# Kernel optimization log

Measured on AMD Instinct MI355X. Metric: run time of the kernel, lower is better.

The kernel has to match this reference:

```python
import jax, jax.numpy as jnp
import numpy as np

H = 16
D_MODEL = 1024
D_K = D_MODEL // H  # 64


def setup_inputs() -> dict:
    key = jax.random.key(0)
    ks = jax.random.split(key, 11)
    B, S = 4, 2048
    scale_in = 1.0 / np.sqrt(D_MODEL)
    inp = {
        "q": jax.random.normal(ks[0], (B, S, D_MODEL), jnp.float32),
        "k": jax.random.normal(ks[1], (B, S, D_MODEL), jnp.float32),
        "v": jax.random.normal(ks[2], (B, S, D_MODEL), jnp.float32),
        # linear params, [in, out] layout (y = x @ W + b)
        "Wq": jax.random.normal(ks[3], (D_MODEL, D_MODEL), jnp.float32) * scale_in,
        "bq": jnp.zeros((D_MODEL,), jnp.float32),
        "Wk": jax.random.normal(ks[4], (D_MODEL, D_K), jnp.float32) * scale_in,
        "bk": jnp.zeros((D_K,), jnp.float32),
        "Wv": jax.random.normal(ks[5], (D_MODEL, D_K), jnp.float32) * scale_in,
        "bv": jnp.zeros((D_K,), jnp.float32),
        "Wo": jax.random.normal(ks[6], (D_MODEL, D_MODEL), jnp.float32) * scale_in,
        "bo": jnp.zeros((D_MODEL,), jnp.float32),
    }
    return inp


def reference(q, k, v, Wq, bq, Wk, bk, Wv, bv, Wo, bo):
    B, S, _ = q.shape
    # projections
    qh = (q @ Wq + bq).reshape(B, S, H, D_K).transpose(0, 2, 1, 3)  # [B,H,S,dk]
    kh = k @ Wk + bk  # [B,S,dk]  single shared K head
    vh = v @ Wv + bv  # [B,S,dk]  single shared V head
    # scaled dot-product attention with broadcast KV head
    scores = jnp.einsum("bhqd,bkd->bhqk", qh, kh) / jnp.sqrt(jnp.float32(D_K))
    p = jax.nn.softmax(scores, axis=-1)  # [B,H,S,S]
    out = jnp.einsum("bhqk,bkd->bhqd", p, vh)  # [B,H,S,dk]
    out = out.transpose(0, 2, 1, 3).reshape(B, S, H * D_K)
    return out @ Wo + bo
```

## Files before the change

kernel.cpp:

```cpp
#include <hip/hip_runtime.h>
#include <hip/hip_bf16.h>

typedef unsigned short u16;
typedef unsigned int u32;
typedef float f32x4 __attribute__((ext_vector_type(4)));
typedef float f32x16 __attribute__((ext_vector_type(16)));
typedef u32 u32x4 __attribute__((ext_vector_type(4)));
typedef __bf16 bf16x8 __attribute__((ext_vector_type(8)));

#define DEVI static __device__ __forceinline__

static constexpr float QK_SCALE = 0.125f * 1.44269504088896340736f;

DEVI u16 bfbits(float f) { __bf16 h = (__bf16)f; return __builtin_bit_cast(u16, h); }
DEVI u32 pk2(float lo, float hi) { return (u32)bfbits(lo) | ((u32)bfbits(hi) << 16); }
DEVI void lswap(u32& a, u32& b) { asm("v_permlane32_swap_b32 %0, %1" : "+v"(a), "+v"(b)); }

typedef unsigned int uint_g __attribute__((address_space(1)));
typedef unsigned int uint_l __attribute__((address_space(3)));

DEVI void gl_lds16(const void* g, void* l) {
  __builtin_amdgcn_global_load_lds((const uint_g*)g, (uint_l*)l, 16, 0, 0);
}

__global__ __launch_bounds__(256) void cvt_f32_bf16(const float* __restrict__ x,
                                                    u16* __restrict__ y, int n4) {
  int i = blockIdx.x * blockDim.x + threadIdx.x;
  int stride = gridDim.x * blockDim.x;
  for (; i < n4; i += stride) {
    float4 v = ((const float4*)x)[i];
    ushort4 o;
    o.x = bfbits(v.x); o.y = bfbits(v.y); o.z = bfbits(v.z); o.w = bfbits(v.w);
    ((ushort4*)y)[i] = o;
  }
}

__global__ __launch_bounds__(256) void wtrans(const float* __restrict__ W,
                                              u16* __restrict__ WT, int K, int N) {
  __shared__ float t[32][33];
  int k0 = blockIdx.x * 32, n0 = blockIdx.y * 32;
  int tx = threadIdx.x & 31, ty = threadIdx.x >> 5;
#pragma unroll
  for (int i = 0; i < 4; ++i)
    t[ty + i * 8][tx] = W[(size_t)(k0 + ty + i * 8) * N + n0 + tx];
  __syncthreads();
#pragma unroll
  for (int i = 0; i < 4; ++i)
    WT[(size_t)(n0 + ty + i * 8) * K + k0 + tx] = bfbits(t[tx][ty + i * 8]);
}

template <int BM, int BN, int WM, int WN, int EPI>
__global__ __launch_bounds__(256) void gemm_bt(const u16* __restrict__ A,
                                               const u16* __restrict__ BT,
                                               const float* __restrict__ bias,
                                               void* __restrict__ out,
                                               int M, int N, int K) {
  constexpr int WROWS = BM / WM, WCOLS = BN / WN;
  constexpr int RT = WROWS / 16, CT = WCOLS / 16;
  __shared__ u16 Alds[BM * 64];
  __shared__ u16 Blds[BN * 64];
  const int tid = threadIdx.x, wave = tid >> 6, lane = tid & 63;
  const int lr = lane & 15, lg = lane >> 4;
  const int wr = wave / WN, wc = wave % WN;
  const int m0 = blockIdx.y * BM, n0 = blockIdx.x * BN;

  f32x4 acc[RT][CT] = {};
  const int nkt = K >> 6;
  for (int kt = 0; kt < nkt; ++kt) {
    const int k0 = kt * 64;
#pragma unroll
    for (int j = 0; j < BM / 32; ++j) {
      int row = j * 32 + (tid >> 3);
      int cel = ((tid & 7) * 8) ^ ((row & 7) << 3);
      gl_lds16(A + (size_t)(m0 + row) * K + k0 + cel,
               (char*)Alds + (j * 256 + wave * 64) * 16);
    }
#pragma unroll
    for (int j = 0; j < BN / 32; ++j) {
      int row = j * 32 + (tid >> 3);
      int cel = ((tid & 7) * 8) ^ ((row & 7) << 3);
      gl_lds16(BT + (size_t)(n0 + row) * K + k0 + cel,
               (char*)Blds + (j * 256 + wave * 64) * 16);
    }
    __syncthreads();
#pragma unroll
    for (int ks = 0; ks < 2; ++ks) {
      bf16x8 af[RT], bfv[CT];
#pragma unroll
      for (int rt = 0; rt < RT; ++rt) {
        int r = wr * WROWS + rt * 16 + lr;
        af[rt] = *(const bf16x8*)&Alds[r * 64 + ((ks * 32 + lg * 8) ^ ((r & 7) << 3))];
      }
#pragma unroll
      for (int ct = 0; ct < CT; ++ct) {
        int r = wc * WCOLS + ct * 16 + lr;
        bfv[ct] = *(const bf16x8*)&Blds[r * 64 + ((ks * 32 + lg * 8) ^ ((r & 7) << 3))];
      }
#pragma unroll
      for (int rt = 0; rt < RT; ++rt)
#pragma unroll
        for (int ct = 0; ct < CT; ++ct)
          acc[rt][ct] = __builtin_amdgcn_mfma_f32_16x16x32_bf16(af[rt], bfv[ct], acc[rt][ct], 0, 0, 0);
    }
    __syncthreads();
  }
#pragma unroll
  for (int ct = 0; ct < CT; ++ct) {
    int n = n0 + wc * WCOLS + ct * 16 + lr;
    float bv = bias[n];
#pragma unroll
    for (int rt = 0; rt < RT; ++rt) {
#pragma unroll
      for (int r = 0; r < 4; ++r) {
        int m = m0 + wr * WROWS + rt * 16 + lg * 4 + r;
        float v = acc[rt][ct][r] + bv;
        if constexpr (EPI == 0) {
          ((float*)out)[(size_t)m * N + n] = v;
        } else if constexpr (EPI == 1) {
          ((u16*)out)[(size_t)m * N + n] = bfbits(v);
        } else if constexpr (EPI == 2) {
          ((u16*)out)[(size_t)m * N + n] = bfbits(v * QK_SCALE);
        } else {
          int bb = m >> 11, s2 = m & 2047;
          ((u16*)out)[((size_t)bb * 64 + n) * 2048 + s2] = bfbits(v);
        }
      }
    }
  }
}

__global__ __launch_bounds__(256, 3) void attn(const u16* __restrict__ qh,
                                               const u16* __restrict__ kh,
                                               const u16* __restrict__ vhT,
                                               u16* __restrict__ att) {
  const int b = blockIdx.z;
  const int tid = threadIdx.x;
  const int wave = tid >> 6, lane = tid & 63;
  const int lq = lane & 31, hi = lane >> 5;
  const int h = blockIdx.y * 4 + wave;
  const int q0 = blockIdx.x * 32;

  __shared__ char KV[2][16384];

  const u16* Qb = qh + (size_t)(b * 2048 + q0) * 1024 + h * 64;
  const u16* Kb = kh + (size_t)b * 2048 * 64;
  const u16* Vb = vhT + (size_t)b * 64 * 2048;

  auto stage = [&](int buf, int kt) {
    char* Lk = KV[buf];
    char* Lv = KV[buf] + 8192;
#pragma unroll
    for (int j = 0; j < 2; ++j) {
      int row = j * 32 + (tid >> 3);
      int cel = ((tid & 7) * 8) ^ ((row & 7) << 3);
      gl_lds16(Kb + (size_t)(kt * 64 + row) * 64 + cel, Lk + j * 4096 + wave * 1024);
      gl_lds16(Vb + (size_t)row * 2048 + kt * 64 + cel, Lv + j * 4096 + wave * 1024);
    }
  };

  bf16x8 qf[4];
#pragma unroll
  for (int ks = 0; ks < 4; ++ks)
    qf[ks] = *(const bf16x8*)(Qb + (size_t)lq * 1024 + ks * 16 + hi * 8);

  f32x16 acc0 = {}, acc1 = {};
  float m = -__builtin_inff(), l = 0.f;

  stage(0, 0);
  __syncthreads();

#pragma unroll 1
  for (int kt = 0; kt < 32; ++kt) {
    const int cur = kt & 1;
    if (kt < 31) stage(cur ^ 1, kt + 1);
    const char* Lk = KV[cur];
    const char* Lv = KV[cur] + 8192;
    f32x16 sc0 = {}, sc1 = {};
    {
      bf16x8 ka[2][4];
#pragma unroll
      for (int t = 0; t < 2; ++t)
#pragma unroll
        for (int ks = 0; ks < 4; ++ks) {
          int row = t * 32 + lq;
          ka[t][ks] = *(const bf16x8*)(Lk + row * 128 + ((ks * 32 + hi * 16) ^ ((row & 7) << 4)));
        }
      __builtin_amdgcn_s_setprio(1);
#pragma unroll
      for (int ks = 0; ks < 4; ++ks)
        sc0 = __builtin_amdgcn_mfma_f32_32x32x16_bf16(ka[0][ks], qf[ks], sc0, 0, 0, 0);
#pragma unroll
      for (int ks = 0; ks < 4; ++ks)
        sc1 = __builtin_amdgcn_mfma_f32_32x32x16_bf16(ka[1][ks], qf[ks], sc1, 0, 0, 0);
      __builtin_amdgcn_s_setprio(0);
    }
    bf16x8 va[2][2][2];
#pragma unroll
    for (int dt = 0; dt < 2; ++dt)
#pragma unroll
      for (int t = 0; t < 2; ++t)
#pragma unroll
        for (int k2 = 0; k2 < 2; ++k2) {
          int row = dt * 32 + lq;
          va[dt][t][k2] = *(const bf16x8*)(Lv + row * 128 + ((t * 64 + k2 * 32 + hi * 16) ^ ((row & 7) << 4)));
        }
    float x8[8], x4[4];
#pragma unroll
    for (int i = 0; i < 8; ++i)
      x8[i] = fmaxf(fmaxf(sc0[i], sc0[i + 8]), fmaxf(sc1[i], sc1[i + 8]));
#pragma unroll
    for (int i = 0; i < 4; ++i) x4[i] = fmaxf(x8[i], x8[i + 4]);
    float mx = fmaxf(fmaxf(x4[0], x4[1]), fmaxf(x4[2], x4[3]));
    mx = fmaxf(mx, __shfl_xor(mx, 32, 64));
    if (!__all(mx <= m + 8.f)) {
      float mn = fmaxf(m, mx);
      float corr = __builtin_amdgcn_exp2f(m - mn);
      m = mn;
      l *= corr;
#pragma unroll
      for (int i = 0; i < 16; ++i) { acc0[i] *= corr; acc1[i] *= corr; }
    }
#pragma unroll
    for (int i = 0; i < 16; ++i) {
      sc0[i] = __builtin_amdgcn_exp2f(sc0[i] - m);
      sc1[i] = __builtin_amdgcn_exp2f(sc1[i] - m);
    }
    float s8[8], s4[4];
#pragma unroll
    for (int i = 0; i < 8; ++i) s8[i] = (sc0[i] + sc0[i + 8]) + (sc1[i] + sc1[i + 8]);
#pragma unroll
    for (int i = 0; i < 4; ++i) s4[i] = s8[i] + s8[i + 4];
    float rs = (s4[0] + s4[1]) + (s4[2] + s4[3]);
    rs += __shfl_xor(rs, 32, 64);
    l += rs;
    u32 w[2][8];
#pragma unroll
    for (int t = 0; t < 2; ++t) {
      const f32x16& s = t ? sc1 : sc0;
      u32 a1 = pk2(s[0], s[1]), a2 = pk2(s[2], s[3]);
      u32 a3 = pk2(s[4], s[5]), a4 = pk2(s[6], s[7]);
      lswap(a1, a3); lswap(a2, a4);
      w[t][0] = a1; w[t][1] = a2; w[t][2] = a3; w[t][3] = a4;
      u32 a5 = pk2(s[8], s[9]), a6 = pk2(s[10], s[11]);
      u32 a7 = pk2(s[12], s[13]), a8 = pk2(s[14], s[15]);
      lswap(a5, a7); lswap(a6, a8);
      w[t][4] = a5; w[t][5] = a6; w[t][6] = a7; w[t][7] = a8;
    }
    __builtin_amdgcn_s_setprio(1);
#pragma unroll
    for (int t = 0; t < 2; ++t)
#pragma unroll
      for (int k2 = 0; k2 < 2; ++k2) {
        u32x4 wv = {w[t][k2 * 4 + 0], w[t][k2 * 4 + 1], w[t][k2 * 4 + 2], w[t][k2 * 4 + 3]};
        bf16x8 pb = __builtin_bit_cast(bf16x8, wv);
        acc0 = __builtin_amdgcn_mfma_f32_32x32x16_bf16(va[0][t][k2], pb, acc0, 0, 0, 0);
        acc1 = __builtin_amdgcn_mfma_f32_32x32x16_bf16(va[1][t][k2], pb, acc1, 0, 0, 0);
      }
    __builtin_amdgcn_s_setprio(0);
    __syncthreads();
  }

  float inv = __builtin_amdgcn_rcpf(l);
  char* ob = (char*)KV + wave * 8192;
#pragma unroll
  for (int dt = 0; dt < 2; ++dt) {
    const f32x16& A = dt ? acc1 : acc0;
#pragma unroll
    for (int i = 0; i < 8; ++i) {
      int r = 2 * i;
      int d = dt * 32 + (r & 3) + 8 * (r >> 2) + 4 * hi;
      u32 pkd = pk2(A[r] * inv, A[r + 1] * inv);
      *(u32*)(ob + lq * 136 + d * 2) = pkd;
    }
  }
  asm volatile("s_waitcnt lgkmcnt(0)" ::: "memory");
  u16* Ob = att + (size_t)(b * 2048 + q0 + lq) * 1024 + h * 64 + hi * 32;
#pragma unroll
  for (int c = 0; c < 8; ++c) {
    uint2 vv = *(const uint2*)(ob + lq * 136 + hi * 64 + c * 8);
    *(uint2*)(Ob + c * 4) = vv;
  }
}

extern "C" void kernel_launch(void* const* d_in, const int* in_sizes, int n_in,
                              void* d_out, int out_size, void* d_ws, size_t ws_size,
                              hipStream_t stream) {
  const float* q  = (const float*)d_in[0];
  const float* k  = (const float*)d_in[1];
  const float* v  = (const float*)d_in[2];
  const float* Wq = (const float*)d_in[3];
  const float* bq = (const float*)d_in[4];
  const float* Wk = (const float*)d_in[5];
  const float* bk = (const float*)d_in[6];
  const float* Wv = (const float*)d_in[7];
  const float* bv = (const float*)d_in[8];
  const float* Wo = (const float*)d_in[9];
  const float* bo = (const float*)d_in[10];
  float* out = (float*)d_out;

  char* ws = (char*)d_ws;
  u16* WqT = (u16*)(ws + 0);
  u16* WoT = (u16*)(ws + 2097152);
  u16* WkT = (u16*)(ws + 4194304);
  u16* WvT = (u16*)(ws + 4325376);
  u16* khb = (u16*)(ws + 4456448);
  u16* vhT = (u16*)(ws + 5505024);
  u16* qhb = (u16*)(ws + 6553600);
  u16* cb0 = (u16*)(ws + 23330816);
  u16* cb1 = (u16*)(ws + 40108032);

  wtrans<<<dim3(32, 32), 256, 0, stream>>>(Wq, WqT, 1024, 1024);
  wtrans<<<dim3(32, 2),  256, 0, stream>>>(Wk, WkT, 1024, 64);
  wtrans<<<dim3(32, 2),  256, 0, stream>>>(Wv, WvT, 1024, 64);
  wtrans<<<dim3(32, 32), 256, 0, stream>>>(Wo, WoT, 1024, 1024);

  cvt_f32_bf16<<<2048, 256, 0, stream>>>(q, cb0, 2097152);
  gemm_bt<128, 128, 2, 2, 2><<<dim3(8, 64), 256, 0, stream>>>(cb0, WqT, bq, (void*)qhb, 8192, 1024, 1024);

  cvt_f32_bf16<<<2048, 256, 0, stream>>>(k, cb0, 2097152);
  gemm_bt<32, 64, 1, 4, 1><<<dim3(1, 256), 256, 0, stream>>>(cb0, WkT, bk, (void*)khb, 8192, 64, 1024);

  cvt_f32_bf16<<<2048, 256, 0, stream>>>(v, cb1, 2097152);
  gemm_bt<32, 64, 1, 4, 3><<<dim3(1, 256), 256, 0, stream>>>(cb1, WvT, bv, (void*)vhT, 8192, 64, 1024);

  attn<<<dim3(64, 4, 4), 256, 0, stream>>>(qhb, khb, vhT, cb1);

  gemm_bt<128, 128, 2, 2, 0><<<dim3(8, 64), 256, 0, stream>>>(cb1, WoT, bo, (void*)out, 8192, 1024, 1024);
}
```

Before: 348.7 us.

## Process 64 query rows per attention wave and fuse input conversions

The attention kernel now gives each wave two 32-row query tiles. Every K/V tile staged in LDS is therefore reused for twice the MFMA work, and the grid is halved. Occupancy drops from 3 to 2 blocks per CU, and register pressure rises with the doubled accumulators. The output store path now writes 16-byte rows through a repacked LDS buffer. The three fp32→bf16 input conversions are merged into one launch, and the workspace buffers are reassigned to match.

```diff
diff --git a/kernel.cpp b/kernel.cpp
--- a/kernel.cpp
+++ b/kernel.cpp
@@ -23,10 +23,18 @@
   __builtin_amdgcn_global_load_lds((const uint_g*)g, (uint_l*)l, 16, 0, 0);
 }
 
-__global__ __launch_bounds__(256) void cvt_f32_bf16(const float* __restrict__ x,
-                                                    u16* __restrict__ y, int n4) {
-  int i = blockIdx.x * blockDim.x + threadIdx.x;
-  int stride = gridDim.x * blockDim.x;
+__global__ __launch_bounds__(256) void cvt3(const float* __restrict__ x0,
+                                            const float* __restrict__ x1,
+                                            const float* __restrict__ x2,
+                                            u16* __restrict__ y0,
+                                            u16* __restrict__ y1,
+                                            u16* __restrict__ y2, int n4) {
+  const int which = blockIdx.x >> 11;
+  const int lb = blockIdx.x & 2047;
+  const float* x = which == 0 ? x0 : (which == 1 ? x1 : x2);
+  u16* y = which == 0 ? y0 : (which == 1 ? y1 : y2);
+  int i = lb * 256 + threadIdx.x;
+  const int stride = 2048 * 256;
   for (; i < n4; i += stride) {
     float4 v = ((const float4*)x)[i];
     ushort4 o;
@@ -129,7 +137,7 @@
   }
 }
 
-__global__ __launch_bounds__(256, 3) void attn(const u16* __restrict__ qh,
+__global__ __launch_bounds__(256, 2) void attn(const u16* __restrict__ qh,
                                                const u16* __restrict__ kh,
                                                const u16* __restrict__ vhT,
                                                u16* __restrict__ att) {
@@ -138,17 +146,17 @@
   const int wave = tid >> 6, lane = tid & 63;
   const int lq = lane & 31, hi = lane >> 5;
   const int h = blockIdx.y * 4 + wave;
-  const int q0 = blockIdx.x * 32;
-
-  __shared__ char KV[2][16384];
+  const int q0 = blockIdx.x * 64;
+
+  __shared__ char SMEM[33792];
 
   const u16* Qb = qh + (size_t)(b * 2048 + q0) * 1024 + h * 64;
   const u16* Kb = kh + (size_t)b * 2048 * 64;
   const u16* Vb = vhT + (size_t)b * 64 * 2048;
 
   auto stage = [&](int buf, int kt) {
-    char* Lk = KV[buf];
-    char* Lv = KV[buf] + 8192;
+    char* Lk = SMEM + buf * 16384;
+    char* Lv = Lk + 8192;
 #pragma unroll
     for (int j = 0; j < 2; ++j) {
       int row = j * 32 + (tid >> 3);
@@ -158,59 +166,25 @@
     }
   };
 
-  bf16x8 qf[4];
-#pragma unroll
-  for (int ks = 0; ks < 4; ++ks)
-    qf[ks] = *(const bf16x8*)(Qb + (size_t)lq * 1024 + ks * 16 + hi * 8);
-
-  f32x16 acc0 = {}, acc1 = {};
-  float m = -__builtin_inff(), l = 0.f;
-
-  stage(0, 0);
-  __syncthreads();
-
-#pragma unroll 1
-  for (int kt = 0; kt < 32; ++kt) {
-    const int cur = kt & 1;
-    if (kt < 31) stage(cur ^ 1, kt + 1);
-    const char* Lk = KV[cur];
-    const char* Lv = KV[cur] + 8192;
-    f32x16 sc0 = {}, sc1 = {};
-    {
-      bf16x8 ka[2][4];
-#pragma unroll
-      for (int t = 0; t < 2; ++t)
-#pragma unroll
-        for (int ks = 0; ks < 4; ++ks) {
-          int row = t * 32 + lq;
-          ka[t][ks] = *(const bf16x8*)(Lk + row * 128 + ((ks * 32 + hi * 16) ^ ((row & 7) << 4)));
-        }
-      __builtin_amdgcn_s_setprio(1);
-#pragma unroll
-      for (int ks = 0; ks < 4; ++ks)
-        sc0 = __builtin_amdgcn_mfma_f32_32x32x16_bf16(ka[0][ks], qf[ks], sc0, 0, 0, 0);
-#pragma unroll
-      for (int ks = 0; ks < 4; ++ks)
-        sc1 = __builtin_amdgcn_mfma_f32_32x32x16_bf16(ka[1][ks], qf[ks], sc1, 0, 0, 0);
-      __builtin_amdgcn_s_setprio(0);
-    }
-    bf16x8 va[2][2][2];
-#pragma unroll
-    for (int dt = 0; dt < 2; ++dt)
-#pragma unroll
-      for (int t = 0; t < 2; ++t)
-#pragma unroll
-        for (int k2 = 0; k2 < 2; ++k2) {
-          int row = dt * 32 + lq;
-          va[dt][t][k2] = *(const bf16x8*)(Lv + row * 128 + ((t * 64 + k2 * 32 + hi * 16) ^ ((row & 7) << 4)));
-        }
-    float x8[8], x4[4];
+  bf16x8 qfA[4], qfB[4];
+#pragma unroll
+  for (int ks = 0; ks < 4; ++ks) {
+    qfA[ks] = *(const bf16x8*)(Qb + (size_t)lq * 1024 + ks * 16 + hi * 8);
+    qfB[ks] = *(const bf16x8*)(Qb + (size_t)(32 + lq) * 1024 + ks * 16 + hi * 8);
+  }
+
+  f32x16 acA0 = {}, acA1 = {}, acB0 = {}, acB1 = {};
+  float mA = -__builtin_inff(), lA = 0.f;
+  float mB = -__builtin_inff(), lB = 0.f;
+
+  auto softmax = [&](f32x16& s0, f32x16& s1, float& m, float& l,
+                     f32x16& a0, f32x16& a1, u32 (&w)[2][8]) {
+    float t8[8];
 #pragma unroll
     for (int i = 0; i < 8; ++i)
-      x8[i] = fmaxf(fmaxf(sc0[i], sc0[i + 8]), fmaxf(sc1[i], sc1[i + 8]));
-#pragma unroll
-    for (int i = 0; i < 4; ++i) x4[i] = fmaxf(x8[i], x8[i + 4]);
-    float mx = fmaxf(fmaxf(x4[0], x4[1]), fmaxf(x4[2], x4[3]));
+      t8[i] = fmaxf(fmaxf(s0[i], s0[i + 8]), fmaxf(s1[i], s1[i + 8]));
+    float mx = fmaxf(fmaxf(fmaxf(t8[0], t8[1]), fmaxf(t8[2], t8[3])),
+                     fmaxf(fmaxf(t8[4], t8[5]), fmaxf(t8[6], t8[7])));
     mx = fmaxf(mx, __shfl_xor(mx, 32, 64));
     if (!__all(mx <= m + 8.f)) {
       float mn = fmaxf(m, mx);
@@ -218,67 +192,120 @@
       m = mn;
       l *= corr;
 #pragma unroll
-      for (int i = 0; i < 16; ++i) { acc0[i] *= corr; acc1[i] *= corr; }
+      for (int i = 0; i < 16; ++i) { a0[i] *= corr; a1[i] *= corr; }
     }
 #pragma unroll
     for (int i = 0; i < 16; ++i) {
-      sc0[i] = __builtin_amdgcn_exp2f(sc0[i] - m);
-      sc1[i] = __builtin_amdgcn_exp2f(sc1[i] - m);
-    }
-    float s8[8], s4[4];
-#pragma unroll
-    for (int i = 0; i < 8; ++i) s8[i] = (sc0[i] + sc0[i + 8]) + (sc1[i] + sc1[i + 8]);
-#pragma unroll
-    for (int i = 0; i < 4; ++i) s4[i] = s8[i] + s8[i + 4];
-    float rs = (s4[0] + s4[1]) + (s4[2] + s4[3]);
+      s0[i] = __builtin_amdgcn_exp2f(s0[i] - m);
+      s1[i] = __builtin_amdgcn_exp2f(s1[i] - m);
+    }
+    f32x4 ps = {};
+#pragma unroll
+    for (int i = 0; i < 4; ++i) {
+      f32x4 u = {s0[i * 4 + 0], s0[i * 4 + 1], s0[i * 4 + 2], s0[i * 4 + 3]};
+      f32x4 v = {s1[i * 4 + 0], s1[i * 4 + 1], s1[i * 4 + 2], s1[i * 4 + 3]};
+      ps += u + v;
+    }
+    float rs = (ps[0] + ps[1]) + (ps[2] + ps[3]);
     rs += __shfl_xor(rs, 32, 64);
     l += rs;
-    u32 w[2][8];
 #pragma unroll
     for (int t = 0; t < 2; ++t) {
-      const f32x16& s = t ? sc1 : sc0;
-      u32 a1 = pk2(s[0], s[1]), a2 = pk2(s[2], s[3]);
-      u32 a3 = pk2(s[4], s[5]), a4 = pk2(s[6], s[7]);
-      lswap(a1, a3); lswap(a2, a4);
-      w[t][0] = a1; w[t][1] = a2; w[t][2] = a3; w[t][3] = a4;
-      u32 a5 = pk2(s[8], s[9]), a6 = pk2(s[10], s[11]);
-      u32 a7 = pk2(s[12], s[13]), a8 = pk2(s[14], s[15]);
-      lswap(a5, a7); lswap(a6, a8);
-      w[t][4] = a5; w[t][5] = a6; w[t][6] = a7; w[t][7] = a8;
-    }
+      const f32x16& s = t ? s1 : s0;
+      u32 a1_ = pk2(s[0], s[1]), a2_ = pk2(s[2], s[3]);
+      u32 a3_ = pk2(s[4], s[5]), a4_ = pk2(s[6], s[7]);
+      lswap(a1_, a3_); lswap(a2_, a4_);
+      w[t][0] = a1_; w[t][1] = a2_; w[t][2] = a3_; w[t][3] = a4_;
+      u32 a5_ = pk2(s[8], s[9]), a6_ = pk2(s[10], s[11]);
+      u32 a7_ = pk2(s[12], s[13]), a8_ = pk2(s[14], s[15]);
+      lswap(a5_, a7_); lswap(a6_, a8_);
+      w[t][4] = a5_; w[t][5] = a6_; w[t][6] = a7_; w[t][7] = a8_;
+    }
+  };
+
+  stage(0, 0);
+  __syncthreads();
+
+#pragma unroll 1
+  for (int kt = 0; kt < 32; ++kt) {
+    const int cur = kt & 1;
+    if (kt < 31) stage(cur ^ 1, kt + 1);
+    const char* Lk = SMEM + cur * 16384;
+    const char* Lv = Lk + 8192;
+    bf16x8 ka[2][4];
+#pragma unroll
+    for (int t = 0; t < 2; ++t)
+#pragma unroll
+      for (int ks = 0; ks < 4; ++ks) {
+        int row = t * 32 + lq;
+        ka[t][ks] = *(const bf16x8*)(Lk + row * 128 + ((ks * 32 + hi * 16) ^ ((row & 7) << 4)));
+      }
+    f32x16 sA0 = {}, sA1 = {}, sB0 = {}, sB1 = {};
     __builtin_amdgcn_s_setprio(1);
 #pragma unroll
+    for (int ks = 0; ks < 4; ++ks) {
+      sA0 = __builtin_amdgcn_mfma_f32_32x32x16_bf16(ka[0][ks], qfA[ks], sA0, 0, 0, 0);
+      sA1 = __builtin_amdgcn_mfma_f32_32x32x16_bf16(ka[1][ks], qfA[ks], sA1, 0, 0, 0);
+      sB0 = __builtin_amdgcn_mfma_f32_32x32x16_bf16(ka[0][ks], qfB[ks], sB0, 0, 0, 0);
+      sB1 = __builtin_amdgcn_mfma_f32_32x32x16_bf16(ka[1][ks], qfB[ks], sB1, 0, 0, 0);
+    }
+    __builtin_amdgcn_s_setprio(0);
+    bf16x8 va[2][2][2];
+#pragma unroll
+    for (int dt = 0; dt < 2; ++dt)
+#pragma unroll
+      for (int t = 0; t < 2; ++t)
+#pragma unroll
+        for (int k2 = 0; k2 < 2; ++k2) {
+          int row = dt * 32 + lq;
+          va[dt][t][k2] = *(const bf16x8*)(Lv + row * 128 + ((t * 64 + k2 * 32 + hi * 16) ^ ((row & 7) << 4)));
+        }
+    u32 wA[2][8], wB[2][8];
+    softmax(sA0, sA1, mA, lA, acA0, acA1, wA);
+    softmax(sB0, sB1, mB, lB, acB0, acB1, wB);
+    __builtin_amdgcn_s_setprio(1);
+#pragma unroll
     for (int t = 0; t < 2; ++t)
 #pragma unroll
       for (int k2 = 0; k2 < 2; ++k2) {
-        u32x4 wv = {w[t][k2 * 4 + 0], w[t][k2 * 4 + 1], w[t][k2 * 4 + 2], w[t][k2 * 4 + 3]};
-        bf16x8 pb = __builtin_bit_cast(bf16x8, wv);
-        acc0 = __builtin_amdgcn_mfma_f32_32x32x16_bf16(va[0][t][k2], pb, acc0, 0, 0, 0);
-        acc1 = __builtin_amdgcn_mfma_f32_32x32x16_bf16(va[1][t][k2], pb, acc1, 0, 0, 0);
+        u32x4 wvA = {wA[t][k2 * 4 + 0], wA[t][k2 * 4 + 1], wA[t][k2 * 4 + 2], wA[t][k2 * 4 + 3]};
+        bf16x8 pA = __builtin_bit_cast(bf16x8, wvA);
+        acA0 = __builtin_amdgcn_mfma_f32_32x32x16_bf16(va[0][t][k2], pA, acA0, 0, 0, 0);
+        acA1 = __builtin_amdgcn_mfma_f32_32x32x16_bf16(va[1][t][k2], pA, acA1, 0, 0, 0);
+        u32x4 wvB = {wB[t][k2 * 4 + 0], wB[t][k2 * 4 + 1], wB[t][k2 * 4 + 2], wB[t][k2 * 4 + 3]};
+        bf16x8 pB = __builtin_bit_cast(bf16x8, wvB);
+        acB0 = __builtin_amdgcn_mfma_f32_32x32x16_bf16(va[0][t][k2], pB, acB0, 0, 0, 0);
+        acB1 = __builtin_amdgcn_mfma_f32_32x32x16_bf16(va[1][t][k2], pB, acB1, 0, 0, 0);
       }
     __builtin_amdgcn_s_setprio(0);
     __syncthreads();
   }
 
-  float inv = __builtin_amdgcn_rcpf(l);
-  char* ob = (char*)KV + wave * 8192;
-#pragma unroll
-  for (int dt = 0; dt < 2; ++dt) {
-    const f32x16& A = dt ? acc1 : acc0;
-#pragma unroll
-    for (int i = 0; i < 8; ++i) {
-      int r = 2 * i;
-      int d = dt * 32 + (r & 3) + 8 * (r >> 2) + 4 * hi;
-      u32 pkd = pk2(A[r] * inv, A[r + 1] * inv);
-      *(u32*)(ob + lq * 136 + d * 2) = pkd;
+  char* ob = SMEM + wave * 8448;
+  {
+    float invA = __builtin_amdgcn_rcpf(lA);
+    float invB = __builtin_amdgcn_rcpf(lB);
+#pragma unroll
+    for (int dt = 0; dt < 2; ++dt) {
+      const f32x16& A0 = dt ? acA1 : acA0;
+      const f32x16& B0 = dt ? acB1 : acB0;
+#pragma unroll
+      for (int i = 0; i < 8; ++i) {
+        int r = 2 * i;
+        int d = dt * 32 + (r & 3) + 8 * (r >> 2) + 4 * hi;
+        *(u32*)(ob + lq * 132 + d * 2) = pk2(A0[r] * invA, A0[r + 1] * invA);
+        *(u32*)(ob + (32 + lq) * 132 + d * 2) = pk2(B0[r] * invB, B0[r + 1] * invB);
+      }
     }
   }
   asm volatile("s_waitcnt lgkmcnt(0)" ::: "memory");
-  u16* Ob = att + (size_t)(b * 2048 + q0 + lq) * 1024 + h * 64 + hi * 32;
-#pragma unroll
-  for (int c = 0; c < 8; ++c) {
-    uint2 vv = *(const uint2*)(ob + lq * 136 + hi * 64 + c * 8);
-    *(uint2*)(Ob + c * 4) = vv;
+  u16* Ob = att + (size_t)(b * 2048 + q0) * 1024 + h * 64;
+#pragma unroll
+  for (int it = 0; it < 8; ++it) {
+    const int r = it * 8 + (lane >> 3);
+    const int c = lane & 7;
+    uint4 vv = *(const uint4*)(ob + r * 132 + c * 16);
+    *(uint4*)(Ob + (size_t)r * 1024 + c * 8) = vv;
   }
 }
 
@@ -305,25 +332,24 @@
   u16* WvT = (u16*)(ws + 4325376);
   u16* khb = (u16*)(ws + 4456448);
   u16* vhT = (u16*)(ws + 5505024);
-  u16* qhb = (u16*)(ws + 6553600);
-  u16* cb0 = (u16*)(ws + 23330816);
-  u16* cb1 = (u16*)(ws + 40108032);
+  u16* S1  = (u16*)(ws + 6553600);
+  u16* S2  = (u16*)(ws + 23330816);
+  u16* S3  = (u16*)(ws + 40108032);
 
   wtrans<<<dim3(32, 32), 256, 0, stream>>>(Wq, WqT, 1024, 1024);
   wtrans<<<dim3(32, 2),  256, 0, stream>>>(Wk, WkT, 1024, 64);
   wtrans<<<dim3(32, 2),  256, 0, stream>>>(Wv, WvT, 1024, 64);
   wtrans<<<dim3(32, 32), 256, 0, stream>>>(Wo, WoT, 1024, 1024);
 
-  cvt_f32_bf16<<<2048, 256, 0, stream>>>(q, cb0, 2097152);
-  gemm_bt<128, 128, 2, 2, 2><<<dim3(8, 64), 256, 0, stream>>>(cb0, WqT, bq, (void*)qhb, 8192, 1024, 1024);
-
-  cvt_f32_bf16<<<2048, 256, 0, stream>>>(k, cb0, 2097152);
-  gemm_bt<32, 64, 1, 4, 1><<<dim3(1, 256), 256, 0, stream>>>(cb0, WkT, bk, (void*)khb, 8192, 64, 1024);
-
-  cvt_f32_bf16<<<2048, 256, 0, stream>>>(v, cb1, 2097152);
-  gemm_bt<32, 64, 1, 4, 3><<<dim3(1, 256), 256, 0, stream>>>(cb1, WvT, bv, (void*)vhT, 8192, 64, 1024);
-
-  attn<<<dim3(64, 4, 4), 256, 0, stream>>>(qhb, khb, vhT, cb1);
-
-  gemm_bt<128, 128, 2, 2, 0><<<dim3(8, 64), 256, 0, stream>>>(cb1, WoT, bo, (void*)out, 8192, 1024, 1024);
-}
+  cvt3<<<6144, 256, 0, stream>>>(q, k, v, S2, S1, S3, 2097152);
+
+  gemm_bt<32, 64, 1, 4, 1><<<dim3(1, 256), 256, 0, stream>>>(S1, WkT, bk, (void*)khb, 8192, 64, 1024);
+
+  gemm_bt<32, 64, 1, 4, 3><<<dim3(1, 256), 256, 0, stream>>>(S3, WvT, bv, (void*)vhT, 8192, 64, 1024);
+
+  gemm_bt<128, 128, 2, 2, 2><<<dim3(8, 64), 256, 0, stream>>>(S2, WqT, bq, (void*)S1, 8192, 1024, 1024);
+
+  attn<<<dim3(32, 4, 4), 256, 0, stream>>>(S1, khb, vhT, S3);
+
+  gemm_bt<128, 128, 2, 2, 0><<<dim3(8, 64), 256, 0, stream>>>(S3, WoT, bo, (void*)out, 8192, 1024, 1024);
+}
```

After: 337.7 us. 1.03x faster.
